# Kernel tuning notes

Hardware: AMD Instinct MI355X
Metric: run time of the kernel (lower is better)

The kernel has to match this reference:

```python
import jax, jax.numpy as jnp
import numpy as np

CHANNELS = 512
NUM_HEADS = 8
GROUPS = 8
EPS = 1e-5


def setup_inputs() -> dict:
    key = jax.random.key(0)
    ks = jax.random.split(key, 7)
    c = CHANNELS
    x = jax.random.normal(ks[0], (32, c, 32, 32), dtype=jnp.float32)
    norm_scale = 1.0 + 0.02 * jax.random.normal(ks[1], (c,), dtype=jnp.float32)
    norm_bias = 0.02 * jax.random.normal(ks[2], (c,), dtype=jnp.float32)
    qkv_w = jax.random.normal(ks[3], (3 * c, c), dtype=jnp.float32) / np.sqrt(c).astype(np.float32)
    qkv_b = 0.01 * jax.random.normal(ks[4], (3 * c,), dtype=jnp.float32)
    proj_w = jax.random.normal(ks[5], (c, c), dtype=jnp.float32) / np.sqrt(c).astype(np.float32)
    proj_b = 0.01 * jax.random.normal(ks[6], (c,), dtype=jnp.float32)
    return {"x": x, "norm_scale": norm_scale, "norm_bias": norm_bias,
            "qkv_w": qkv_w, "qkv_b": qkv_b, "proj_w": proj_w, "proj_b": proj_b}


def reference(x, norm_scale, norm_bias, qkv_w, qkv_b, proj_w, proj_b):
    b, c, h, w = x.shape
    heads = NUM_HEADS
    d = c // heads  # head dim
    # GroupNorm(8, c): normalize over (c//groups, h, w) per group
    xg = x.reshape(b, GROUPS, -1)
    mean = xg.mean(axis=-1, keepdims=True)
    var = xg.var(axis=-1, keepdims=True)
    xn = ((xg - mean) * jax.lax.rsqrt(var + EPS)).reshape(b, c, h, w)
    xn = xn * norm_scale[:, None, None] + norm_bias[:, None, None]
    # 1x1 conv == per-pixel GEMM over channels
    qkv = jnp.einsum('bchw,oc->bohw', xn, qkv_w) + qkv_b[:, None, None]
    q, k, v = jnp.split(qkv, 3, axis=1)  # each [b, c, h, w]
    q = q.reshape(b, heads, d, h * w)
    k = k.reshape(b, heads, d, h * w)
    v = v.reshape(b, heads, d, h * w)
    # scores: [b, heads, hw, hw]
    attn = jnp.einsum('bhdn,bhdm->bhnm', q, k) * (d ** -0.5)
    attn = jax.nn.softmax(attn, axis=-1)
    out = jnp.einsum('bhnm,bhdm->bhdn', attn, v).reshape(b, c, h, w)
    out = jnp.einsum('bchw,oc->bohw', out, proj_w) + proj_b[:, None, None]
    return out + x
```

## Files before the change

kernel.cpp:

```cpp
#include <hip/hip_runtime.h>
#include <stdint.h>

typedef float  f32x4  __attribute__((ext_vector_type(4)));
typedef float  f32x16 __attribute__((ext_vector_type(16)));
typedef __bf16 bf16x8 __attribute__((ext_vector_type(8)));
typedef unsigned int   u32;
typedef unsigned int   u32x4v __attribute__((ext_vector_type(4)));
typedef unsigned short u16;

#define DEVI static __device__ __forceinline__

DEVI void gload16(void* lds, const void* g) {
  __builtin_amdgcn_global_load_lds((const __attribute__((address_space(1))) u32*)g,
                                   (__attribute__((address_space(3))) u32*)lds, 16, 0, 0);
}
DEVI f32x4 mfma16(bf16x8 a, bf16x8 b, f32x4 c) {
  return __builtin_amdgcn_mfma_f32_16x16x32_bf16(a, b, c, 0, 0, 0);
}
DEVI f32x16 mfma32(bf16x8 a, bf16x8 b, f32x16 c) {
  return __builtin_amdgcn_mfma_f32_32x32x16_bf16(a, b, c, 0, 0, 0);
}
DEVI u16 f2bf(float f) {
  u32 u = __builtin_bit_cast(u32, f);
  return (u16)((u + 0x7FFFu + ((u >> 16) & 1u)) >> 16);
}
DEVI u32 cvtpk(float lo, float hi) {
  u32 r;
  asm("v_cvt_pk_bf16_f32 %0, %1, %2" : "=v"(r) : "v"(lo), "v"(hi));
  return r;
}
DEVI bf16x8 mkfrag(u32 a, u32 b, u32 c, u32 d) {
  u32x4v u = {a, b, c, d};
  return __builtin_bit_cast(bf16x8, u);
}
#if __has_builtin(__builtin_amdgcn_exp2f)
DEVI float exp2fast(float x) { return __builtin_amdgcn_exp2f(x); }
#else
DEVI float exp2fast(float x) { return exp2f(x); }
#endif

__global__ __launch_bounds__(256) void k_gnstats(const float* __restrict__ x,
                                                 float* __restrict__ meanr) {
  const int bg = blockIdx.x;
  const float4* p4 = (const float4*)(x + (size_t)bg * 65536);
  const int t = threadIdx.x;
  float s = 0.f, ss = 0.f;
  for (int i = t; i < 16384; i += 256) {
    float4 v = p4[i];
    s  += v.x + v.y + v.z + v.w;
    ss += v.x*v.x + v.y*v.y + v.z*v.z + v.w*v.w;
  }
  for (int off = 32; off; off >>= 1) { s += __shfl_down(s, off); ss += __shfl_down(ss, off); }
  __shared__ float sa[4], sb[4];
  const int w = t >> 6;
  if ((t & 63) == 0) { sa[w] = s; sb[w] = ss; }
  __syncthreads();
  if (t == 0) {
    float S = sa[0]+sa[1]+sa[2]+sa[3], SS = sb[0]+sb[1]+sb[2]+sb[3];
    float mean = S * (1.f/65536.f);
    float var  = SS * (1.f/65536.f) - mean*mean;
    meanr[2*bg]   = mean;
    meanr[2*bg+1] = rsqrtf(var + 1e-5f);
  }
}

__global__ __launch_bounds__(256) void k_cvt(const float* __restrict__ a,
                                             u16* __restrict__ o, int n) {
  int i = blockIdx.x * 256 + threadIdx.x;
  const int stride = gridDim.x * 256;
  for (; i < n; i += stride) o[i] = f2bf(a[i]);
}

__global__ __launch_bounds__(256) void k_norm_t(
    const float* __restrict__ x, const float* __restrict__ meanr,
    const float* __restrict__ scale, const float* __restrict__ bias,
    u16* __restrict__ xnT) {
  __shared__ __align__(16) char T[8192];
  const int t = threadIdx.x;
  const int nt = blockIdx.x, ct = blockIdx.y, b = blockIdx.z;
  const int n0 = nt*64, c0 = ct*64;
  const float mean = meanr[2*(b*8 + ct)];
  const float rstd = meanr[2*(b*8 + ct) + 1];
  const int n_l = t & 63;
  const float* xb = x + ((size_t)b*512 + c0)*1024 + n0;
  #pragma unroll
  for (int i = 0; i < 16; i++) {
    int c_l = i*4 + (t>>6);
    float xv = xb[(size_t)c_l*1024 + n_l];
    float val = (xv - mean)*rstd*scale[c0+c_l] + bias[c0+c_l];
    *(u16*)(T + n_l*128 + ((c_l*2) ^ ((n_l&7)<<4))) = f2bf(val);
  }
  __syncthreads();
  u16* outp = xnT + ((size_t)b*1024 + n0)*512 + c0;
  #pragma unroll
  for (int i = 0; i < 2; i++) {
    int idx = i*256 + t;
    int n_ = idx >> 3, s = idx & 7;
    uint4 val = *(const uint4*)(T + n_*128 + ((s ^ (n_&7))<<4));
    *(uint4*)((char*)outp + (size_t)n_*1024 + s*16) = val;
  }
}

template<int MODE>
__global__ __launch_bounds__(256) void k_gemm(
    const u16* __restrict__ A, const u16* __restrict__ Bt,
    const float* __restrict__ bias, const float* __restrict__ xres,
    u16* __restrict__ oq, u16* __restrict__ ok, u16* __restrict__ ov,
    float* __restrict__ out) {
  __shared__ __align__(16) char lds[65536];
  const int t = threadIdx.x;
  const int wv = t >> 6, ln = t & 63;
  const int wr = wv >> 1, wc = wv & 1;
  const int b  = blockIdx.z;
  const int n0 = blockIdx.x * 128;
  const int m0 = blockIdx.y * 128;
  const u16* Bb = Bt + (size_t)b * (1024*512);

  f32x4 acc[4][4];
  #pragma unroll
  for (int i = 0; i < 4; i++)
    #pragma unroll
    for (int j = 0; j < 4; j++) acc[i][j] = f32x4{0.f,0.f,0.f,0.f};

  const int srow = ln >> 3, ssl = ln & 7;
  const int csw  = ssl ^ (srow & 7);

  auto stage = [&](int buf, int kb) {
    char* base = lds + (buf << 15);
    #pragma unroll
    for (int i = 0; i < 4; i++) {
      int row = wv*32 + i*8 + srow;
      gload16(base + (wv*32 + i*8)*128,
              (const char*)A  + ((size_t)(m0+row)*512 + kb*64)*2 + csw*16);
      gload16(base + 16384 + (wv*32 + i*8)*128,
              (const char*)Bb + ((size_t)(n0+row)*512 + kb*64)*2 + csw*16);
    }
  };

  stage(0, 0);
  __syncthreads();

  for (int kb = 0; kb < 8; kb++) {
    if (kb < 7) stage((kb + 1) & 1, kb + 1);
    const char* cb = lds + ((kb & 1) << 15);
    #pragma unroll
    for (int kf = 0; kf < 2; kf++) {
      bf16x8 af[4], bfr[4];
      #pragma unroll
      for (int mi = 0; mi < 4; mi++) {
        int row = wr*64 + mi*16 + (ln & 15);
        af[mi] = *(const bf16x8*)(cb + row*128 + ((kf*64 + ((ln>>4)<<4)) ^ ((row&7)<<4)));
      }
      #pragma unroll
      for (int ni = 0; ni < 4; ni++) {
        int row = wc*64 + ni*16 + (ln & 15);
        bfr[ni] = *(const bf16x8*)(cb + 16384 + row*128 + ((kf*64 + ((ln>>4)<<4)) ^ ((row&7)<<4)));
      }
      __builtin_amdgcn_s_setprio(1);
      #pragma unroll
      for (int mi = 0; mi < 4; mi++)
        #pragma unroll
        for (int ni = 0; ni < 4; ni++)
          acc[mi][ni] = mfma16(af[mi], bfr[ni], acc[mi][ni]);
      __builtin_amdgcn_s_setprio(0);
    }
    __syncthreads();
  }

  if constexpr (MODE == 0) {
    if (m0 >= 1024) {
      #pragma unroll
      for (int mi = 0; mi < 4; mi++) {
        #pragma unroll
        for (int r = 0; r < 4; r++) {
          int o_l = wr*64 + mi*16 + ((ln>>4)<<2) + r;
          float bia = bias[m0 + o_l];
          size_t rowoff = ((size_t)b*512 + (m0-1024) + o_l)*1024 + n0 + wc*64 + (ln & 15);
          #pragma unroll
          for (int ni = 0; ni < 4; ni++)
            ov[rowoff + ni*16] = f2bf(acc[mi][ni][r] + bia);
        }
      }
    } else {
      const bool isq = (m0 < 512);
      const float sq = isq ? 0.18033688f : 1.0f;
      u16* dstb = isq ? oq : ok;
      const int mloc = isq ? m0 : (m0 - 512);
      #pragma unroll
      for (int mi = 0; mi < 4; mi++) {
        #pragma unroll
        for (int r = 0; r < 4; r++) {
          int o_l = wr*64 + mi*16 + ((ln>>4)<<2) + r;
          float bia = bias[m0 + o_l];
          #pragma unroll
          for (int ni = 0; ni < 4; ni++) {
            int n_l = wc*64 + ni*16 + (ln & 15);
            *(u16*)(lds + n_l*256 + ((o_l*2) ^ ((n_l&7)<<4))) =
                f2bf((acc[mi][ni][r] + bia) * sq);
          }
        }
      }
      __syncthreads();
      const int h0 = mloc >> 6;
      #pragma unroll
      for (int i = 0; i < 8; i++) {
        int idx = i*256 + t;
        int n_ = idx >> 4, s = idx & 15;
        uint4 val = *(const uint4*)(lds + n_*256 + ((s ^ (n_&7))<<4));
        u16* dst = dstb + ((size_t)(b*8 + h0 + (s>>3))*1024 + (n0 + n_))*64 + (s&7)*8;
        *(uint4*)dst = val;
      }
    }
  } else {
    #pragma unroll
    for (int mi = 0; mi < 4; mi++) {
      #pragma unroll
      for (int r = 0; r < 4; r++) {
        int o_l = wr*64 + mi*16 + ((ln>>4)<<2) + r;
        float bia = bias[m0 + o_l];
        size_t rowoff = ((size_t)b*512 + m0 + o_l)*1024 + n0 + wc*64 + (ln & 15);
        #pragma unroll
        for (int ni = 0; ni < 4; ni++)
          out[rowoff + ni*16] = acc[mi][ni][r] + bia + xres[rowoff + ni*16];
      }
    }
  }
}

__global__ __launch_bounds__(512, 4) void k_attn(
    const u16* __restrict__ qT, const u16* __restrict__ kT,
    const u16* __restrict__ v, u16* __restrict__ aoT) {
  __shared__ __align__(16) char lds[65536];
  const int t = threadIdx.x, wv = t >> 6, ln = t & 63;
  const int l31 = ln & 31, hi = ln >> 5;
  const int qt = blockIdx.x, h = blockIdx.y, b = blockIdx.z;
  const size_t bh = (size_t)(b*8 + h);
  const int q0 = qt*256 + wv*32;
  const char* qp = (const char*)qT + (bh*1024 + q0)*128;
  const char* kp = (const char*)kT + bh*1024*128;
  const char* vp = (const char*)v  + bh*64*2048;

  const int srow = ln >> 3;
  const int csw16 = ((ln & 7) ^ srow) << 4;
  const int rsw = (l31 & 7) << 4;
  const int grow = wv*8 + srow;

  auto stageChunk = [&](char* base, int mc) {
    gload16(base + wv*1024,         kp + (size_t)(mc*128 + grow)*128 + csw16);
    gload16(base + 8192 + wv*1024,  kp + (size_t)(mc*128 + 64 + grow)*128 + csw16);
    gload16(base + 16384 + wv*1024, vp + (size_t)grow*2048 + mc*256 + csw16);
    gload16(base + 24576 + wv*1024, vp + (size_t)grow*2048 + mc*256 + 128 + csw16);
  };

  stageChunk(lds, 0);

  bf16x8 qf[4];
  #pragma unroll
  for (int ks = 0; ks < 4; ks++)
    qf[ks] = *(const bf16x8*)(qp + (size_t)l31*128 + ks*32 + hi*16);

  f32x16 zv;
  #pragma unroll
  for (int i = 0; i < 16; i++) zv[i] = 0.f;

  f32x16 o0, o1;
  #pragma unroll
  for (int i = 0; i < 16; i++) { o0[i] = 0.f; o1[i] = 0.f; }
  float M = -1e30f, L = 0.f;

  auto qk = [&](const char* Kl, f32x16& s0, f32x16& s1) {
    __builtin_amdgcn_s_setprio(1);
    {
      int col = (hi*16) ^ rsw;
      bf16x8 k0 = *(const bf16x8*)(Kl + (size_t)l31*128 + col);
      bf16x8 k1 = *(const bf16x8*)(Kl + (size_t)(32 + l31)*128 + col);
      s0 = mfma32(k0, qf[0], zv);
      s1 = mfma32(k1, qf[0], zv);
    }
    #pragma unroll
    for (int ks = 1; ks < 4; ks++) {
      int col = (ks*32 + hi*16) ^ rsw;
      bf16x8 k0 = *(const bf16x8*)(Kl + (size_t)l31*128 + col);
      bf16x8 k1 = *(const bf16x8*)(Kl + (size_t)(32 + l31)*128 + col);
      s0 = mfma32(k0, qf[ks], s0);
      s1 = mfma32(k1, qf[ks], s1);
    }
    __builtin_amdgcn_s_setprio(0);
  };

  auto sm = [&](f32x16& s0, f32x16& s1, bf16x8* pf) {
    float m8[8];
    #pragma unroll
    for (int i = 0; i < 8; i++)
      m8[i] = fmaxf(fmaxf(s0[2*i], s0[2*i+1]), fmaxf(s1[2*i], s1[2*i+1]));
    float m4a = fmaxf(m8[0], m8[1]), m4b = fmaxf(m8[2], m8[3]);
    float m4c = fmaxf(m8[4], m8[5]), m4d = fmaxf(m8[6], m8[7]);
    float cm = fmaxf(fmaxf(m4a, m4b), fmaxf(m4c, m4d));
    cm = fmaxf(cm, __shfl_xor(cm, 32));
    if (!__all(cm <= M + 11.f)) {
      float nm = fmaxf(M, cm);
      float al = exp2fast(M - nm);
      M = nm;
      #pragma unroll
      for (int i = 0; i < 16; i++) { o0[i] *= al; o1[i] *= al; }
      L *= al;
    }
    #pragma unroll
    for (int i = 0; i < 16; i++) {
      s0[i] = exp2fast(s0[i] - M);
      s1[i] = exp2fast(s1[i] - M);
    }
    float r8[8];
    #pragma unroll
    for (int i = 0; i < 8; i++)
      r8[i] = (s0[2*i] + s0[2*i+1]) + (s1[2*i] + s1[2*i+1]);
    float r4a = r8[0] + r8[1], r4b = r8[2] + r8[3];
    float r4c = r8[4] + r8[5], r4d = r8[6] + r8[7];
    L += (r4a + r4b) + (r4c + r4d);

    u32 x0 = cvtpk(s0[0],  s0[1]),  x1 = cvtpk(s0[2],  s0[3]);
    u32 x2 = cvtpk(s0[4],  s0[5]),  x3 = cvtpk(s0[6],  s0[7]);
    u32 x4 = cvtpk(s0[8],  s0[9]),  x5 = cvtpk(s0[10], s0[11]);
    u32 x6 = cvtpk(s0[12], s0[13]), x7 = cvtpk(s0[14], s0[15]);
    u32 y0 = cvtpk(s1[0],  s1[1]),  y1 = cvtpk(s1[2],  s1[3]);
    u32 y2 = cvtpk(s1[4],  s1[5]),  y3 = cvtpk(s1[6],  s1[7]);
    u32 y4 = cvtpk(s1[8],  s1[9]),  y5 = cvtpk(s1[10], s1[11]);
    u32 y6 = cvtpk(s1[12], s1[13]), y7 = cvtpk(s1[14], s1[15]);
    u32 e0 = (u32)__shfl_xor((int)(hi ? x0 : x2), 32);
    u32 e1 = (u32)__shfl_xor((int)(hi ? x1 : x3), 32);
    u32 e2 = (u32)__shfl_xor((int)(hi ? x4 : x6), 32);
    u32 e3 = (u32)__shfl_xor((int)(hi ? x5 : x7), 32);
    u32 f0 = (u32)__shfl_xor((int)(hi ? y0 : y2), 32);
    u32 f1 = (u32)__shfl_xor((int)(hi ? y1 : y3), 32);
    u32 f2 = (u32)__shfl_xor((int)(hi ? y4 : y6), 32);
    u32 f3 = (u32)__shfl_xor((int)(hi ? y5 : y7), 32);
    pf[0] = hi ? mkfrag(e0, e1, x2, x3) : mkfrag(x0, x1, e0, e1);
    pf[1] = hi ? mkfrag(e2, e3, x6, x7) : mkfrag(x4, x5, e2, e3);
    pf[2] = hi ? mkfrag(f0, f1, y2, y3) : mkfrag(y0, y1, f0, f1);
    pf[3] = hi ? mkfrag(f2, f3, y6, y7) : mkfrag(y4, y5, f2, f3);
  };

  auto pv = [&](const char* Vl, const bf16x8* pf) {
    __builtin_amdgcn_s_setprio(1);
    #pragma unroll
    for (int s = 0; s < 4; s++) {
      int col = (s*32 + hi*16) ^ rsw;
      bf16x8 v0 = *(const bf16x8*)(Vl + (size_t)l31*128 + col);
      bf16x8 v1 = *(const bf16x8*)(Vl + (size_t)(32 + l31)*128 + col);
      o0 = mfma32(v0, pf[s], o0);
      o1 = mfma32(v1, pf[s], o1);
    }
    __builtin_amdgcn_s_setprio(0);
  };

  __syncthreads();

  for (int mc = 0; mc < 8; mc++) {
    char* cb = lds + ((mc & 1) << 15);
    if (mc < 7) stageChunk(lds + (((mc + 1) & 1) << 15), mc + 1);
    f32x16 sa0, sa1, sb0, sb1;
    bf16x8 pfA[4], pfB[4];
    qk(cb, sa0, sa1);
    sm(sa0, sa1, pfA);
    qk(cb + 8192, sb0, sb1);
    pv(cb + 16384, pfA);
    sm(sb0, sb1, pfB);
    pv(cb + 24576, pfB);
    __syncthreads();
  }

  L += __shfl_xor(L, 32);
  float inv = 1.f / L;
  u16* dst = aoT + ((size_t)(b*1024 + q0 + l31))*512 + h*64;
  #pragma unroll
  for (int qd = 0; qd < 4; qd++) {
    uint2 val;
    val.x = cvtpk(o0[4*qd+0]*inv, o0[4*qd+1]*inv);
    val.y = cvtpk(o0[4*qd+2]*inv, o0[4*qd+3]*inv);
    *(uint2*)(dst + qd*8 + hi*4) = val;
  }
  #pragma unroll
  for (int qd = 0; qd < 4; qd++) {
    uint2 val;
    val.x = cvtpk(o1[4*qd+0]*inv, o1[4*qd+1]*inv);
    val.y = cvtpk(o1[4*qd+2]*inv, o1[4*qd+3]*inv);
    *(uint2*)(dst + 32 + qd*8 + hi*4) = val;
  }
}

extern "C" void kernel_launch(void* const* d_in, const int* in_sizes, int n_in,
                              void* d_out, int out_size, void* d_ws, size_t ws_size,
                              hipStream_t stream) {
  const float* x     = (const float*)d_in[0];
  const float* nsc   = (const float*)d_in[1];
  const float* nbi   = (const float*)d_in[2];
  const float* qkvw  = (const float*)d_in[3];
  const float* qkvb  = (const float*)d_in[4];
  const float* projw = (const float*)d_in[5];
  const float* projb = (const float*)d_in[6];
  float* out = (float*)d_out;

  char* ws = (char*)d_ws;
  float* meanr = (float*)ws;
  u16* qkvwb  = (u16*)(ws + 2048);
  u16* projwb = (u16*)(ws + 2048 + 1572864);
  char* p = ws + 2048 + 1572864 + 524288;
  u16* qT  = (u16*)p; p += 33554432;
  u16* kTb = (u16*)p; p += 33554432;
  u16* vb  = (u16*)p; p += 33554432;
  u16* xnT = (u16*)p;
  u16* aoT = xnT;

  k_gnstats<<<256, 256, 0, stream>>>(x, meanr);
  k_cvt<<<768, 256, 0, stream>>>(qkvw, qkvwb, 1536*512);
  k_cvt<<<256, 256, 0, stream>>>(projw, projwb, 512*512);
  k_norm_t<<<dim3(16, 8, 32), 256, 0, stream>>>(x, meanr, nsc, nbi, xnT);
  k_gemm<0><<<dim3(8, 12, 32), 256, 0, stream>>>(qkvwb, xnT, qkvb, nullptr,
                                                 qT, kTb, vb, nullptr);
  k_attn<<<dim3(4, 8, 32), 512, 0, stream>>>(qT, kTb, vb, aoT);
  k_gemm<1><<<dim3(8, 4, 32), 256, 0, stream>>>(projwb, aoT, projb, x,
                                                nullptr, nullptr, nullptr, out);
}
```

Measured before the change: 245.3 us.

## Process two 32-query tiles per wave in attention to reuse K/V fragments

Each wave now handles 64 queries as two 32-row tiles, so every K and V fragment read from LDS feeds two MFMAs instead of one. The grid's query dimension is halved and the launch-bounds occupancy hint is dropped. This halves the LDS reads per MFMA and halves the total K/V staging traffic across blocks. The cost is more accumulator registers per thread (four 16-wide output accumulators plus two sets of score registers), lower occupancy, and half as many blocks (512) to cover the GPU.

```diff
diff --git a/kernel.cpp b/kernel.cpp
--- a/kernel.cpp
+++ b/kernel.cpp
@@ -227,7 +227,7 @@
   }
 }
 
-__global__ __launch_bounds__(512, 4) void k_attn(
+__global__ __launch_bounds__(512) void k_attn(
     const u16* __restrict__ qT, const u16* __restrict__ kT,
     const u16* __restrict__ v, u16* __restrict__ aoT) {
   __shared__ __align__(16) char lds[65536];
@@ -235,7 +235,7 @@
   const int l31 = ln & 31, hi = ln >> 5;
   const int qt = blockIdx.x, h = blockIdx.y, b = blockIdx.z;
   const size_t bh = (size_t)(b*8 + h);
-  const int q0 = qt*256 + wv*32;
+  const int q0 = qt*512 + wv*64;
   const char* qp = (const char*)qT + (bh*1024 + q0)*128;
   const char* kp = (const char*)kT + bh*1024*128;
   const char* vp = (const char*)v  + bh*64*2048;
@@ -254,41 +254,37 @@
 
   stageChunk(lds, 0);
 
-  bf16x8 qf[4];
-  #pragma unroll
-  for (int ks = 0; ks < 4; ks++)
-    qf[ks] = *(const bf16x8*)(qp + (size_t)l31*128 + ks*32 + hi*16);
-
-  f32x16 zv;
-  #pragma unroll
-  for (int i = 0; i < 16; i++) zv[i] = 0.f;
-
-  f32x16 o0, o1;
-  #pragma unroll
-  for (int i = 0; i < 16; i++) { o0[i] = 0.f; o1[i] = 0.f; }
-  float M = -1e30f, L = 0.f;
-
-  auto qk = [&](const char* Kl, f32x16& s0, f32x16& s1) {
+  bf16x8 qfA[4], qfB[4];
+  #pragma unroll
+  for (int ks = 0; ks < 4; ks++) {
+    qfA[ks] = *(const bf16x8*)(qp + (size_t)l31*128 + ks*32 + hi*16);
+    qfB[ks] = *(const bf16x8*)(qp + (size_t)(32 + l31)*128 + ks*32 + hi*16);
+  }
+
+  f32x16 oA0, oA1, oB0, oB1;
+  #pragma unroll
+  for (int i = 0; i < 16; i++) { oA0[i] = 0.f; oA1[i] = 0.f; oB0[i] = 0.f; oB1[i] = 0.f; }
+  float MA = -1e30f, LA = 0.f, MB = -1e30f, LB = 0.f;
+
+  auto qk_dual = [&](const char* Kl, f32x16& a0, f32x16& a1, f32x16& b0, f32x16& b1) {
+    #pragma unroll
+    for (int i = 0; i < 16; i++) { a0[i] = 0.f; a1[i] = 0.f; b0[i] = 0.f; b1[i] = 0.f; }
     __builtin_amdgcn_s_setprio(1);
-    {
-      int col = (hi*16) ^ rsw;
-      bf16x8 k0 = *(const bf16x8*)(Kl + (size_t)l31*128 + col);
-      bf16x8 k1 = *(const bf16x8*)(Kl + (size_t)(32 + l31)*128 + col);
-      s0 = mfma32(k0, qf[0], zv);
-      s1 = mfma32(k1, qf[0], zv);
-    }
-    #pragma unroll
-    for (int ks = 1; ks < 4; ks++) {
+    #pragma unroll
+    for (int ks = 0; ks < 4; ks++) {
       int col = (ks*32 + hi*16) ^ rsw;
       bf16x8 k0 = *(const bf16x8*)(Kl + (size_t)l31*128 + col);
       bf16x8 k1 = *(const bf16x8*)(Kl + (size_t)(32 + l31)*128 + col);
-      s0 = mfma32(k0, qf[ks], s0);
-      s1 = mfma32(k1, qf[ks], s1);
+      a0 = mfma32(k0, qfA[ks], a0);
+      a1 = mfma32(k1, qfA[ks], a1);
+      b0 = mfma32(k0, qfB[ks], b0);
+      b1 = mfma32(k1, qfB[ks], b1);
     }
     __builtin_amdgcn_s_setprio(0);
   };
 
-  auto sm = [&](f32x16& s0, f32x16& s1, bf16x8* pf) {
+  auto sm = [&](f32x16& s0, f32x16& s1, float& M, float& L,
+                f32x16& o0, f32x16& o1, bf16x8* pf) {
     float m8[8];
     #pragma unroll
     for (int i = 0; i < 8; i++)
@@ -340,15 +336,17 @@
     pf[3] = hi ? mkfrag(f2, f3, y6, y7) : mkfrag(y4, y5, f2, f3);
   };
 
-  auto pv = [&](const char* Vl, const bf16x8* pf) {
+  auto pv_dual = [&](const char* Vl, const bf16x8* pfA, const bf16x8* pfB) {
     __builtin_amdgcn_s_setprio(1);
     #pragma unroll
     for (int s = 0; s < 4; s++) {
       int col = (s*32 + hi*16) ^ rsw;
       bf16x8 v0 = *(const bf16x8*)(Vl + (size_t)l31*128 + col);
       bf16x8 v1 = *(const bf16x8*)(Vl + (size_t)(32 + l31)*128 + col);
-      o0 = mfma32(v0, pf[s], o0);
-      o1 = mfma32(v1, pf[s], o1);
+      oA0 = mfma32(v0, pfA[s], oA0);
+      oA1 = mfma32(v1, pfA[s], oA1);
+      oB0 = mfma32(v0, pfB[s], oB0);
+      oB1 = mfma32(v1, pfB[s], oB1);
     }
     __builtin_amdgcn_s_setprio(0);
   };
@@ -358,33 +356,40 @@
   for (int mc = 0; mc < 8; mc++) {
     char* cb = lds + ((mc & 1) << 15);
     if (mc < 7) stageChunk(lds + (((mc + 1) & 1) << 15), mc + 1);
-    f32x16 sa0, sa1, sb0, sb1;
-    bf16x8 pfA[4], pfB[4];
-    qk(cb, sa0, sa1);
-    sm(sa0, sa1, pfA);
-    qk(cb + 8192, sb0, sb1);
-    pv(cb + 16384, pfA);
-    sm(sb0, sb1, pfB);
-    pv(cb + 24576, pfB);
+    #pragma unroll
+    for (int half = 0; half < 2; half++) {
+      const char* Kl = cb + half*8192;
+      const char* Vl = cb + 16384 + half*8192;
+      f32x16 sa0, sa1, sb0, sb1;
+      bf16x8 pfA[4], pfB[4];
+      qk_dual(Kl, sa0, sa1, sb0, sb1);
+      sm(sa0, sa1, MA, LA, oA0, oA1, pfA);
+      sm(sb0, sb1, MB, LB, oB0, oB1, pfB);
+      pv_dual(Vl, pfA, pfB);
+    }
     __syncthreads();
   }
 
-  L += __shfl_xor(L, 32);
-  float inv = 1.f / L;
-  u16* dst = aoT + ((size_t)(b*1024 + q0 + l31))*512 + h*64;
+  LA += __shfl_xor(LA, 32);
+  LB += __shfl_xor(LB, 32);
+  float invA = 1.f / LA, invB = 1.f / LB;
+  u16* dstA = aoT + ((size_t)(b*1024 + q0 + l31))*512 + h*64;
+  u16* dstB = dstA + 32*512;
   #pragma unroll
   for (int qd = 0; qd < 4; qd++) {
     uint2 val;
-    val.x = cvtpk(o0[4*qd+0]*inv, o0[4*qd+1]*inv);
-    val.y = cvtpk(o0[4*qd+2]*inv, o0[4*qd+3]*inv);
-    *(uint2*)(dst + qd*8 + hi*4) = val;
-  }
-  #pragma unroll
-  for (int qd = 0; qd < 4; qd++) {
-    uint2 val;
-    val.x = cvtpk(o1[4*qd+0]*inv, o1[4*qd+1]*inv);
-    val.y = cvtpk(o1[4*qd+2]*inv, o1[4*qd+3]*inv);
-    *(uint2*)(dst + 32 + qd*8 + hi*4) = val;
+    val.x = cvtpk(oA0[4*qd+0]*invA, oA0[4*qd+1]*invA);
+    val.y = cvtpk(oA0[4*qd+2]*invA, oA0[4*qd+3]*invA);
+    *(uint2*)(dstA + qd*8 + hi*4) = val;
+    val.x = cvtpk(oA1[4*qd+0]*invA, oA1[4*qd+1]*invA);
+    val.y = cvtpk(oA1[4*qd+2]*invA, oA1[4*qd+3]*invA);
+    *(uint2*)(dstA + 32 + qd*8 + hi*4) = val;
+    val.x = cvtpk(oB0[4*qd+0]*invB, oB0[4*qd+1]*invB);
+    val.y = cvtpk(oB0[4*qd+2]*invB, oB0[4*qd+3]*invB);
+    *(uint2*)(dstB + qd*8 + hi*4) = val;
+    val.x = cvtpk(oB1[4*qd+0]*invB, oB1[4*qd+1]*invB);
+    val.y = cvtpk(oB1[4*qd+2]*invB, oB1[4*qd+3]*invB);
+    *(uint2*)(dstB + 32 + qd*8 + hi*4) = val;
   }
 }
 
@@ -417,7 +422,7 @@
   k_norm_t<<<dim3(16, 8, 32), 256, 0, stream>>>(x, meanr, nsc, nbi, xnT);
   k_gemm<0><<<dim3(8, 12, 32), 256, 0, stream>>>(qkvwb, xnT, qkvb, nullptr,
                                                  qT, kTb, vb, nullptr);
-  k_attn<<<dim3(4, 8, 32), 512, 0, stream>>>(qT, kTb, vb, aoT);
+  k_attn<<<dim3(2, 8, 32), 512, 0, stream>>>(qT, kTb, vb, aoT);
   k_gemm<1><<<dim3(8, 4, 32), 256, 0, stream>>>(projwb, aoT, projb, x,
                                                 nullptr, nullptr, nullptr, out);
 }
```

Result: slower. 257.8 us (+5.1%).

## Fuse GroupNorm statistics and normalize-transpose into one kernel per group

Applied to the files above, without the earlier changes.

Replaces the separate stats kernel and the normalize/transpose kernel with one 1024-thread block per (batch, group). The block computes the mean and rstd, then normalizes and transposes its 64 channels into the bf16 layout. This removes a launch and the workspace round trip for the stats, and the second read of x may be served by L2. The trade-off is a grid of only 256 blocks of 1024 threads, each reading 256KB twice, which lowers parallelism compared with the previous 4096-block normalize kernel.

```diff
diff --git a/kernel.cpp b/kernel.cpp
--- a/kernel.cpp
+++ b/kernel.cpp
@@ -39,28 +39,61 @@
 DEVI float exp2fast(float x) { return exp2f(x); }
 #endif
 
-__global__ __launch_bounds__(256) void k_gnstats(const float* __restrict__ x,
-                                                 float* __restrict__ meanr) {
-  const int bg = blockIdx.x;
-  const float4* p4 = (const float4*)(x + (size_t)bg * 65536);
+__global__ __launch_bounds__(1024) void k_gn_norm_t(
+    const float* __restrict__ x, const float* __restrict__ scale,
+    const float* __restrict__ bias, u16* __restrict__ xnT) {
+  const int g = blockIdx.x, b = blockIdx.y;
+  const float* xg = x + ((size_t)(b*8 + g)) * 65536;
   const int t = threadIdx.x;
+
   float s = 0.f, ss = 0.f;
-  for (int i = t; i < 16384; i += 256) {
-    float4 v = p4[i];
+  const float4* p4 = (const float4*)xg;
+  #pragma unroll
+  for (int i = 0; i < 16; i++) {
+    float4 v = p4[t + i*1024];
     s  += v.x + v.y + v.z + v.w;
     ss += v.x*v.x + v.y*v.y + v.z*v.z + v.w*v.w;
   }
+  #pragma unroll
   for (int off = 32; off; off >>= 1) { s += __shfl_down(s, off); ss += __shfl_down(ss, off); }
-  __shared__ float sa[4], sb[4];
-  const int w = t >> 6;
-  if ((t & 63) == 0) { sa[w] = s; sb[w] = ss; }
+  __shared__ float sa[16], sb[16];
+  __shared__ float stats[2];
+  if ((t & 63) == 0) { sa[t >> 6] = s; sb[t >> 6] = ss; }
   __syncthreads();
   if (t == 0) {
-    float S = sa[0]+sa[1]+sa[2]+sa[3], SS = sb[0]+sb[1]+sb[2]+sb[3];
+    float S = 0.f, SS = 0.f;
+    #pragma unroll
+    for (int i = 0; i < 16; i++) { S += sa[i]; SS += sb[i]; }
     float mean = S * (1.f/65536.f);
     float var  = SS * (1.f/65536.f) - mean*mean;
-    meanr[2*bg]   = mean;
-    meanr[2*bg+1] = rsqrtf(var + 1e-5f);
+    stats[0] = mean;
+    stats[1] = rsqrtf(var + 1e-5f);
+  }
+  __syncthreads();
+  const float mean = stats[0], rstd = stats[1];
+
+  __shared__ __align__(16) char T[4][8192];
+  const int grp = t >> 8, lt = t & 255;
+  const int n_l = lt & 63;
+  for (int it = 0; it < 4; it++) {
+    const int n0 = (it*4 + grp) * 64;
+    #pragma unroll
+    for (int i = 0; i < 16; i++) {
+      int c_l = i*4 + (lt >> 6);
+      float xv = xg[(size_t)c_l*1024 + n0 + n_l];
+      float val = (xv - mean)*rstd*scale[g*64 + c_l] + bias[g*64 + c_l];
+      *(u16*)(T[grp] + n_l*128 + ((c_l*2) ^ ((n_l&7)<<4))) = f2bf(val);
+    }
+    __syncthreads();
+    u16* outp = xnT + ((size_t)b*1024 + n0)*512 + g*64;
+    #pragma unroll
+    for (int i = 0; i < 2; i++) {
+      int idx = i*256 + lt;
+      int n_ = idx >> 3, sl = idx & 7;
+      uint4 val = *(const uint4*)(T[grp] + n_*128 + ((sl ^ (n_&7))<<4));
+      *(uint4*)((char*)outp + (size_t)n_*1024 + sl*16) = val;
+    }
+    __syncthreads();
   }
 }
 
@@ -69,36 +102,6 @@
   int i = blockIdx.x * 256 + threadIdx.x;
   const int stride = gridDim.x * 256;
   for (; i < n; i += stride) o[i] = f2bf(a[i]);
-}
-
-__global__ __launch_bounds__(256) void k_norm_t(
-    const float* __restrict__ x, const float* __restrict__ meanr,
-    const float* __restrict__ scale, const float* __restrict__ bias,
-    u16* __restrict__ xnT) {
-  __shared__ __align__(16) char T[8192];
-  const int t = threadIdx.x;
-  const int nt = blockIdx.x, ct = blockIdx.y, b = blockIdx.z;
-  const int n0 = nt*64, c0 = ct*64;
-  const float mean = meanr[2*(b*8 + ct)];
-  const float rstd = meanr[2*(b*8 + ct) + 1];
-  const int n_l = t & 63;
-  const float* xb = x + ((size_t)b*512 + c0)*1024 + n0;
-  #pragma unroll
-  for (int i = 0; i < 16; i++) {
-    int c_l = i*4 + (t>>6);
-    float xv = xb[(size_t)c_l*1024 + n_l];
-    float val = (xv - mean)*rstd*scale[c0+c_l] + bias[c0+c_l];
-    *(u16*)(T + n_l*128 + ((c_l*2) ^ ((n_l&7)<<4))) = f2bf(val);
-  }
-  __syncthreads();
-  u16* outp = xnT + ((size_t)b*1024 + n0)*512 + c0;
-  #pragma unroll
-  for (int i = 0; i < 2; i++) {
-    int idx = i*256 + t;
-    int n_ = idx >> 3, s = idx & 7;
-    uint4 val = *(const uint4*)(T + n_*128 + ((s ^ (n_&7))<<4));
-    *(uint4*)((char*)outp + (size_t)n_*1024 + s*16) = val;
-  }
 }
 
 template<int MODE>
@@ -401,7 +404,6 @@
   float* out = (float*)d_out;
 
   char* ws = (char*)d_ws;
-  float* meanr = (float*)ws;
   u16* qkvwb  = (u16*)(ws + 2048);
   u16* projwb = (u16*)(ws + 2048 + 1572864);
   char* p = ws + 2048 + 1572864 + 524288;
@@ -411,10 +413,9 @@
   u16* xnT = (u16*)p;
   u16* aoT = xnT;
 
-  k_gnstats<<<256, 256, 0, stream>>>(x, meanr);
   k_cvt<<<768, 256, 0, stream>>>(qkvw, qkvwb, 1536*512);
   k_cvt<<<256, 256, 0, stream>>>(projw, projwb, 512*512);
-  k_norm_t<<<dim3(16, 8, 32), 256, 0, stream>>>(x, meanr, nsc, nbi, xnT);
+  k_gn_norm_t<<<dim3(8, 32), 1024, 0, stream>>>(x, nsc, nbi, xnT);
   k_gemm<0><<<dim3(8, 12, 32), 256, 0, stream>>>(qkvwb, xnT, qkvb, nullptr,
                                                  qT, kTb, vb, nullptr);
   k_attn<<<dim3(4, 8, 32), 512, 0, stream>>>(qT, kTb, vb, aoT);
```

Result: faster. 236.9 us (-3.4%).
